# Optimization experiments

Measured on AMD Instinct MI355X. Metric: run time of the kernel, lower is better.

Reference implementation:

```python
import jax, jax.numpy as jnp
import numpy as np

B, C, D, H, W = 8, 1, 160, 160, 160
SPATIAL_AXES = (2, 3, 4)  # axial, coronal, sagittal map to dims D, H, W


def setup_inputs() -> dict:
    key = jax.random.key(0)
    k1, _ = jax.random.split(key)
    x = jax.random.normal(k1, (B, C, D, H, W), dtype=jnp.float32)
    log_sigma = jnp.zeros((3,), dtype=jnp.float32)  # log(initial_sigma=1.0)
    return {"x": x, "log_sigma": log_sigma}


def reference(x, log_sigma):
    # For each spatial axis: adjacent-slice diff, squared distance summed over
    # channel + remaining spatial dims (per batch, per slice-pair), RBF kernel,
    # then -mean over (batch, slice-pairs). Equivalent to the original
    # sum_i(-mean_b(k_i)) / (n_slices - 1) since mean is linear.
    sigma = jnp.exp(log_sigma)
    total = jnp.float32(0.0)
    for i, ax in enumerate(SPATIAL_AXES):
        d = jnp.diff(x, axis=ax)  # [B, C, ...] with S-1 along ax
        reduce_dims = tuple(a for a in range(5) if a not in (0, ax))
        sq = jnp.sum(d * d, axis=reduce_dims)  # [B, S-1]
        k = jnp.exp(-sq / (2.0 * sigma[i] ** 2))
        total = total + (-jnp.mean(k))
    return total / jnp.float32(len(SPATIAL_AXES))
```

## Files before the change

### kernel.cpp

```cpp
#include <hip/hip_runtime.h>


constexpr int Wd = 160;
constexpr int SLICE = 160 * 160;
constexpr long BSTRIDE = 160L * 25600;
constexpr int NB = 8;
constexpr int NPAIR = 159;
constexpr int WS_FLOATS = 3 * NB * NPAIR;

__global__ void zero_ws_kernel(float* __restrict__ ws) {
    int i = blockIdx.x * 256 + threadIdx.x;
    if (i < WS_FLOATS) ws[i] = 0.f;
}

__global__ __launch_bounds__(320) void diff3_kernel(const float* __restrict__ x,
                                                    float* __restrict__ ws) {
    __shared__ __align__(16) float buf[2][17 * Wd];
    __shared__ float accD[10];
    __shared__ float accH[16];
    __shared__ float accW[160];

    const int t = threadIdx.x;
    const int bid = blockIdx.x;
    const int b = bid / 160;
    const int rem = bid % 160;
    const int s = rem / 10;
    const int hc = rem % 10;
    const int h0 = hc * 16;
    const int d0 = s * 10;
    const int nsl = (s < 15) ? 11 : 10;

    const int fw = t % 40;
    const int r1 = t / 40;
    const int r2 = r1 + 8;
    const bool halo = (t < 40) && (hc < 9);

    if (t < 10)  accD[t] = 0.f;
    if (t < 16)  accH[t] = 0.f;
    if (t < 160) accW[t] = 0.f;

    const float* xb = x + (size_t)b * BSTRIDE + (size_t)h0 * Wd + (size_t)fw * 4;

    float4 pv1, pv2;
    float aH1 = 0.f, aH2 = 0.f;
    float aW0 = 0.f, aW1 = 0.f, aW2 = 0.f, aW3 = 0.f;

    for (int it = 0; it < nsl; ++it) {
        const float* sp = xb + (size_t)(d0 + it) * SLICE;
        const float4 v1 = *(const float4*)(sp + r1 * Wd);
        const float4 v2 = *(const float4*)(sp + r2 * Wd);
        float4 v3;
        if (halo) v3 = *(const float4*)(sp + 16 * Wd);

        float* Bf = buf[it & 1];
        *(float4*)(Bf + r1 * Wd + fw * 4) = v1;
        *(float4*)(Bf + r2 * Wd + fw * 4) = v2;
        if (halo) *(float4*)(Bf + 16 * Wd + fw * 4) = v3;
        __syncthreads();

        if (it > 0) {
            float dx0 = v1.x - pv1.x, dx1 = v1.y - pv1.y, dx2 = v1.z - pv1.z, dx3 = v1.w - pv1.w;
            float dy0 = v2.x - pv2.x, dy1 = v2.y - pv2.y, dy2 = v2.z - pv2.z, dy3 = v2.w - pv2.w;
            float dd = dx0*dx0 + dx1*dx1 + dx2*dx2 + dx3*dx3
                     + dy0*dy0 + dy1*dy1 + dy2*dy2 + dy3*dy3;
            for (int off = 32; off > 0; off >>= 1) dd += __shfl_down(dd, off, 64);
            if ((t & 63) == 0) atomicAdd(&accD[it - 1], dd);
        }
        pv1 = v1; pv2 = v2;

        if (it < 10) {
            {
                float dw;
                dw = v1.y - v1.x; aW0 += dw * dw;
                dw = v1.z - v1.y; aW1 += dw * dw;
                dw = v1.w - v1.z; aW2 += dw * dw;
                if (fw < 39) { dw = Bf[r1 * Wd + fw * 4 + 4] - v1.w; aW3 += dw * dw; }
                if (h0 + r1 < 159) {
                    const float4 hb = *(const float4*)(Bf + (r1 + 1) * Wd + fw * 4);
                    float e0 = hb.x - v1.x, e1 = hb.y - v1.y, e2 = hb.z - v1.z, e3 = hb.w - v1.w;
                    aH1 += e0*e0 + e1*e1 + e2*e2 + e3*e3;
                }
            }
            {
                float dw;
                dw = v2.y - v2.x; aW0 += dw * dw;
                dw = v2.z - v2.y; aW1 += dw * dw;
                dw = v2.w - v2.z; aW2 += dw * dw;
                if (fw < 39) { dw = Bf[r2 * Wd + fw * 4 + 4] - v2.w; aW3 += dw * dw; }
                if (h0 + r2 < 159) {
                    const float4 hb = *(const float4*)(Bf + (r2 + 1) * Wd + fw * 4);
                    float e0 = hb.x - v2.x, e1 = hb.y - v2.y, e2 = hb.z - v2.z, e3 = hb.w - v2.w;
                    aH2 += e0*e0 + e1*e1 + e2*e2 + e3*e3;
                }
            }
        }
    }

    atomicAdd(&accH[r1], aH1);
    atomicAdd(&accH[r2], aH2);
    atomicAdd(&accW[fw * 4 + 0], aW0);
    atomicAdd(&accW[fw * 4 + 1], aW1);
    atomicAdd(&accW[fw * 4 + 2], aW2);
    if (fw < 39) atomicAdd(&accW[fw * 4 + 3], aW3);
    __syncthreads();

    float* wsD = ws;
    float* wsH = ws + NB * NPAIR;
    float* wsW = ws + 2 * NB * NPAIR;
    const int nd = nsl - 1;
    if (t < nd) atomicAdd(&wsD[b * NPAIR + d0 + t], accD[t]);
    if (t >= 32 && t < 48) {
        int r = t - 32;
        if (h0 + r < 159) atomicAdd(&wsH[b * NPAIR + h0 + r], accH[r]);
    }
    if (t >= 64 && t < 64 + 159) {
        int k = t - 64;
        atomicAdd(&wsW[b * NPAIR + k], accW[k]);
    }
}

__global__ __launch_bounds__(256) void finalize_kernel(const float* __restrict__ ws,
                                                       const float* __restrict__ log_sigma,
                                                       float* __restrict__ out) {
    __shared__ float ssum;
    const int t = threadIdx.x;
    if (t == 0) ssum = 0.f;
    __syncthreads();

    const float f0 = -0.5f * expf(-2.f * log_sigma[0]);
    const float f1 = -0.5f * expf(-2.f * log_sigma[1]);
    const float f2 = -0.5f * expf(-2.f * log_sigma[2]);

    float acc = 0.f;
    const int n = NB * NPAIR;
    for (int i = t; i < n; i += 256) acc += expf(ws[i] * f0);
    for (int i = t; i < n; i += 256) acc += expf(ws[n + i] * f1);
    for (int i = t; i < n; i += 256) acc += expf(ws[2 * n + i] * f2);

    for (int off = 32; off > 0; off >>= 1) acc += __shfl_down(acc, off, 64);
    if ((t & 63) == 0) atomicAdd(&ssum, acc);
    __syncthreads();
    if (t == 0) out[0] = -ssum / (float)(3 * NB * NPAIR);
}

extern "C" void kernel_launch(void* const* d_in, const int* in_sizes, int n_in,
                              void* d_out, int out_size, void* d_ws, size_t ws_size,
                              hipStream_t stream) {
    const float* x = (const float*)d_in[0];
    const float* log_sigma = (const float*)d_in[1];
    float* out = (float*)d_out;
    float* ws = (float*)d_ws;

    zero_ws_kernel<<<(WS_FLOATS + 255) / 256, 256, 0, stream>>>(ws);
    diff3_kernel<<<8 * 10 * 16, 320, 0, stream>>>(x, ws);
    finalize_kernel<<<1, 256, 0, stream>>>(ws, log_sigma, out);
}
```

Baseline: 207.6 us.

## Software-pipeline slice loads by prefetching the next D slice into registers

The slice loop is restructured so the next depth slice is loaded from global memory into registers before the current slice's W/H/D differences are computed, then written to the alternate shared buffer afterwards. The aim is to hide global-load latency behind the arithmetic instead of stalling right after each load. The extra D pair from the eleventh slice is handled in an epilogue. Register pressure rises from holding the next slice's values, and the boundary conditions are rewritten, with hOK2 replacing the per-row H checks.

```diff
diff --git a/kernel.cpp b/kernel.cpp
--- a/kernel.cpp
+++ b/kernel.cpp
@@ -28,72 +28,96 @@
     const int hc = rem % 10;
     const int h0 = hc * 16;
     const int d0 = s * 10;
-    const int nsl = (s < 15) ? 11 : 10;
+    const bool lastSeg = (s == 15);
 
     const int fw = t % 40;
     const int r1 = t / 40;
     const int r2 = r1 + 8;
     const bool halo = (t < 40) && (hc < 9);
+    const bool hOK2 = !(hc == 9 && r1 == 7);
 
     if (t < 10)  accD[t] = 0.f;
     if (t < 16)  accH[t] = 0.f;
     if (t < 160) accW[t] = 0.f;
 
-    const float* xb = x + (size_t)b * BSTRIDE + (size_t)h0 * Wd + (size_t)fw * 4;
+    const float* xb = x + (size_t)b * BSTRIDE + (size_t)d0 * SLICE
+                        + (size_t)h0 * Wd + (size_t)fw * 4;
 
-    float4 pv1, pv2;
+    float4 c1 = *(const float4*)(xb + r1 * Wd);
+    float4 c2 = *(const float4*)(xb + r2 * Wd);
+    float4 c3;
+    if (halo) c3 = *(const float4*)(xb + 16 * Wd);
+    {
+        float* Bf = buf[0];
+        *(float4*)(Bf + r1 * Wd + fw * 4) = c1;
+        *(float4*)(Bf + r2 * Wd + fw * 4) = c2;
+        if (halo) *(float4*)(Bf + 16 * Wd + fw * 4) = c3;
+    }
+    __syncthreads();
+
+    float4 p1, p2;
     float aH1 = 0.f, aH2 = 0.f;
     float aW0 = 0.f, aW1 = 0.f, aW2 = 0.f, aW3 = 0.f;
 
-    for (int it = 0; it < nsl; ++it) {
-        const float* sp = xb + (size_t)(d0 + it) * SLICE;
-        const float4 v1 = *(const float4*)(sp + r1 * Wd);
-        const float4 v2 = *(const float4*)(sp + r2 * Wd);
-        float4 v3;
-        if (halo) v3 = *(const float4*)(sp + 16 * Wd);
+    for (int it = 0; it < 10; ++it) {
+        const bool hasNext = (it < 9) || !lastSeg;
+        float4 n1, n2, n3;
+        const float* sp = xb + (size_t)(it + 1) * SLICE;
+        if (hasNext) {
+            n1 = *(const float4*)(sp + r1 * Wd);
+            n2 = *(const float4*)(sp + r2 * Wd);
+            if (halo && it < 9) n3 = *(const float4*)(sp + 16 * Wd);
+        }
 
-        float* Bf = buf[it & 1];
-        *(float4*)(Bf + r1 * Wd + fw * 4) = v1;
-        *(float4*)(Bf + r2 * Wd + fw * 4) = v2;
-        if (halo) *(float4*)(Bf + 16 * Wd + fw * 4) = v3;
-        __syncthreads();
-
+        const float* Bf = buf[it & 1];
+        float dw;
+        dw = c1.y - c1.x; aW0 += dw * dw;
+        dw = c1.z - c1.y; aW1 += dw * dw;
+        dw = c1.w - c1.z; aW2 += dw * dw;
+        dw = c2.y - c2.x; aW0 += dw * dw;
+        dw = c2.z - c2.y; aW1 += dw * dw;
+        dw = c2.w - c2.z; aW2 += dw * dw;
+        if (fw < 39) {
+            float b1 = Bf[r1 * Wd + fw * 4 + 4]; dw = b1 - c1.w; aW3 += dw * dw;
+            float b2 = Bf[r2 * Wd + fw * 4 + 4]; dw = b2 - c2.w; aW3 += dw * dw;
+        }
+        {
+            const float4 hb = *(const float4*)(Bf + (r1 + 1) * Wd + fw * 4);
+            float e0 = hb.x - c1.x, e1 = hb.y - c1.y, e2 = hb.z - c1.z, e3 = hb.w - c1.w;
+            aH1 += e0 * e0 + e1 * e1 + e2 * e2 + e3 * e3;
+        }
+        if (hOK2) {
+            const float4 hb = *(const float4*)(Bf + (r2 + 1) * Wd + fw * 4);
+            float e0 = hb.x - c2.x, e1 = hb.y - c2.y, e2 = hb.z - c2.z, e3 = hb.w - c2.w;
+            aH2 += e0 * e0 + e1 * e1 + e2 * e2 + e3 * e3;
+        }
         if (it > 0) {
-            float dx0 = v1.x - pv1.x, dx1 = v1.y - pv1.y, dx2 = v1.z - pv1.z, dx3 = v1.w - pv1.w;
-            float dy0 = v2.x - pv2.x, dy1 = v2.y - pv2.y, dy2 = v2.z - pv2.z, dy3 = v2.w - pv2.w;
+            float dx0 = c1.x - p1.x, dx1 = c1.y - p1.y, dx2 = c1.z - p1.z, dx3 = c1.w - p1.w;
+            float dy0 = c2.x - p2.x, dy1 = c2.y - p2.y, dy2 = c2.z - p2.z, dy3 = c2.w - p2.w;
             float dd = dx0*dx0 + dx1*dx1 + dx2*dx2 + dx3*dx3
                      + dy0*dy0 + dy1*dy1 + dy2*dy2 + dy3*dy3;
             for (int off = 32; off > 0; off >>= 1) dd += __shfl_down(dd, off, 64);
             if ((t & 63) == 0) atomicAdd(&accD[it - 1], dd);
         }
-        pv1 = v1; pv2 = v2;
 
-        if (it < 10) {
-            {
-                float dw;
-                dw = v1.y - v1.x; aW0 += dw * dw;
-                dw = v1.z - v1.y; aW1 += dw * dw;
-                dw = v1.w - v1.z; aW2 += dw * dw;
-                if (fw < 39) { dw = Bf[r1 * Wd + fw * 4 + 4] - v1.w; aW3 += dw * dw; }
-                if (h0 + r1 < 159) {
-                    const float4 hb = *(const float4*)(Bf + (r1 + 1) * Wd + fw * 4);
-                    float e0 = hb.x - v1.x, e1 = hb.y - v1.y, e2 = hb.z - v1.z, e3 = hb.w - v1.w;
-                    aH1 += e0*e0 + e1*e1 + e2*e2 + e3*e3;
-                }
-            }
-            {
-                float dw;
-                dw = v2.y - v2.x; aW0 += dw * dw;
-                dw = v2.z - v2.y; aW1 += dw * dw;
-                dw = v2.w - v2.z; aW2 += dw * dw;
-                if (fw < 39) { dw = Bf[r2 * Wd + fw * 4 + 4] - v2.w; aW3 += dw * dw; }
-                if (h0 + r2 < 159) {
-                    const float4 hb = *(const float4*)(Bf + (r2 + 1) * Wd + fw * 4);
-                    float e0 = hb.x - v2.x, e1 = hb.y - v2.y, e2 = hb.z - v2.z, e3 = hb.w - v2.w;
-                    aH2 += e0*e0 + e1*e1 + e2*e2 + e3*e3;
-                }
-            }
+        p1 = c1; p2 = c2;
+        if (hasNext) { c1 = n1; c2 = n2; }
+        if (it < 9) {
+            float* Nf = buf[(it + 1) & 1];
+            *(float4*)(Nf + r1 * Wd + fw * 4) = n1;
+            *(float4*)(Nf + r2 * Wd + fw * 4) = n2;
+            if (halo) *(float4*)(Nf + 16 * Wd + fw * 4) = n3;
+            __syncthreads();
         }
+    }
+
+    if (!lastSeg) {
+        float dx0 = c1.x - p1.x, dx1 = c1.y - p1.y, dx2 = c1.z - p1.z, dx3 = c1.w - p1.w;
+        float dy0 = c2.x - p2.x, dy1 = c2.y - p2.y, dy2 = c2.z - p2.z, dy3 = c2.w - p2.w;
+        float dd = dx0*dx0 + dx1*dx1 + dx2*dx2 + dx3*dx3
+                 + dy0*dy0 + dy1*dy1 + dy2*dy2 + dy3*dy3;
+        for (int off = 32; off > 0; off >>= 1) dd += __shfl_down(dd, off, 64);
+        if ((t & 63) == 0) atomicAdd(&accD[9], dd);
     }
 
     atomicAdd(&accH[r1], aH1);
@@ -107,7 +131,7 @@
     float* wsD = ws;
     float* wsH = ws + NB * NPAIR;
     float* wsW = ws + 2 * NB * NPAIR;
-    const int nd = nsl - 1;
+    const int nd = lastSeg ? 9 : 10;
     if (t < nd) atomicAdd(&wsD[b * NPAIR + d0 + t], accD[t]);
     if (t >= 32 && t < 48) {
         int r = t - 32;
```

Measured after the change: 220.8 us. 1.06x slower.
